# Kernel optimization log

Measured on AMD Instinct MI355X. Metric: run time of the kernel, lower is better.

Reference implementation:

```python
import jax, jax.numpy as jnp
import numpy as np

INV_SQRT2 = 0.7071067811865476  # 1/sqrt(2), orthonormal Haar
N_LEVELS = 3


def setup_inputs() -> dict:
    key = jax.random.key(0)
    ks = jax.random.split(key, 5)
    B, S, D = 16, 4096, 512
    x = jax.random.normal(ks[0], (B, S, D), dtype=jnp.float32)
    sizes = [256, 128, 64]  # detail-band sizes for 3-level DWT of 512
    Wd0 = jax.random.normal(ks[1], (sizes[0], sizes[0]), dtype=jnp.float32) * 0.02
    Wd1 = jax.random.normal(ks[2], (sizes[1], sizes[1]), dtype=jnp.float32) * 0.02
    Wd2 = jax.random.normal(ks[3], (sizes[2], sizes[2]), dtype=jnp.float32) * 0.02
    Wa = jax.random.normal(ks[4], (sizes[2], sizes[2]), dtype=jnp.float32) * 0.02
    return {
        'x': x,
        'Wd0': Wd0, 'bd0': jnp.zeros((sizes[0],), jnp.float32),
        'Wd1': Wd1, 'bd1': jnp.zeros((sizes[1],), jnp.float32),
        'Wd2': Wd2, 'bd2': jnp.zeros((sizes[2],), jnp.float32),
        'Wa': Wa, 'ba': jnp.zeros((sizes[2],), jnp.float32),
    }


def reference(x, Wd0, bd0, Wd1, bd1, Wd2, bd2, Wa, ba):
    # Multi-level Haar DWT along the feature axis.
    details = []
    a = x
    for _ in range(N_LEVELS):
        e = a[..., 0::2]
        o = a[..., 1::2]
        details.append((e - o) * INV_SQRT2)  # detail coefficients
        a = (e + o) * INV_SQRT2              # approximation coefficients

    # Per-level small linear transforms (torch Linear: y = x @ W.T + b).
    Wds, bds = [Wd0, Wd1, Wd2], [bd0, bd1, bd2]
    details = [details[i] @ Wds[i].T + bds[i] for i in range(N_LEVELS)]
    a = a @ Wa.T + ba

    # Inverse Haar DWT (orthonormal): even=(a+d)/sqrt2, odd=(a-d)/sqrt2, interleave.
    for i in reversed(range(N_LEVELS)):
        d = details[i]
        e = (a + d) * INV_SQRT2
        o = (a - d) * INV_SQRT2
        a = jnp.stack([e, o], axis=-1).reshape(a.shape[:-1] + (a.shape[-1] * 2,))
    return a
```

## Files before the change

### kernel.cpp

```cpp
#include <hip/hip_runtime.h>
#include <stdint.h>

typedef float  f32x4  __attribute__((ext_vector_type(4)));
typedef short  bf16x8 __attribute__((ext_vector_type(8)));
typedef int    i32x4  __attribute__((ext_vector_type(4)));
typedef unsigned int u32x2 __attribute__((ext_vector_type(2)));

#define C1f 0.70710678118654752f
#define C2f 0.5f
#define C3f 0.35355339059327373f

#define NT 1024
#define CH 32
#define RB 1040
#define RPB 256
#define NCHUNK (RPB/CH)

__device__ __forceinline__ unsigned int f2b(float f) {
    unsigned int u; __builtin_memcpy(&u, &f, 4);
    u += 0x7fffu + ((u >> 16) & 1u);
    return u >> 16;
}
__device__ __forceinline__ unsigned int pack2(float lo, float hi) {
    return f2b(lo) | (f2b(hi) << 16);
}
__device__ __forceinline__ bf16x8 cast8(i32x4 v) {
    bf16x8 r; __builtin_memcpy(&r, &v, 16); return r;
}

__device__ __forceinline__ void lds_barrier() {
    asm volatile("s_waitcnt lgkmcnt(0)" ::: "memory");
    __builtin_amdgcn_s_barrier();
    __builtin_amdgcn_sched_barrier(0);
}

__device__ __forceinline__ bf16x8 g_frag(int o, int i0,
        const float* __restrict__ W0, const float* __restrict__ W1,
        const float* __restrict__ W2, const float* __restrict__ Wa)
{
    const float s0o = (o & 1) ? -1.f : 1.f;
    const float s1o = ((o >> 1) & 1) ? -1.f : 1.f;
    const float s2o = ((o >> 2) & 1) ? -1.f : 1.f;
    const float4 w0 = *(const float4*)(W0 + (o >> 1) * 256 + (i0 >> 1));
    const float2 w1 = *(const float2*)(W1 + (o >> 2) * 128 + (i0 >> 2));
    const float  w2 = W2[(o >> 3) * 64 + (i0 >> 3)];
    const float  wa = Wa[(o >> 3) * 64 + (i0 >> 3)];
    const float base = 0.125f * wa;
    const float c2   = 0.125f * s2o * w2;
    const float c1   = 0.25f  * s1o;
    const float c0   = 0.5f   * s0o;
    const float w0a[4] = { w0.x, w0.y, w0.z, w0.w };
    const float w1a[2] = { w1.x, w1.y };
    float g[8];
    #pragma unroll
    for (int e = 0; e < 8; ++e) {
        const float t2 = ((e >> 2) & 1) ? -c2 : c2;
        const float t1 = (((e >> 1) & 1) ? -c1 : c1) * w1a[e >> 2];
        const float t0 = ((e & 1) ? -c0 : c0) * w0a[e >> 1];
        g[e] = base + t2 + t1 + t0;
    }
    i32x4 p = { (int)pack2(g[0],g[1]), (int)pack2(g[2],g[3]),
                (int)pack2(g[4],g[5]), (int)pack2(g[6],g[7]) };
    return cast8(p);
}

__global__ void prep(const float* __restrict__ W0, const float* __restrict__ b0,
                     const float* __restrict__ W1, const float* __restrict__ b1,
                     const float* __restrict__ W2, const float* __restrict__ b2,
                     const float* __restrict__ Wa, const float* __restrict__ ba,
                     unsigned short* __restrict__ ws)
{
    const int gid  = blockIdx.x * 256 + threadIdx.x;
    const int blob = gid >> 6, lane = gid & 63;
    const int otg  = blob >> 4, ks = blob & 15;
    const int o  = otg * 16 + (lane & 15);
    const int i0 = ks * 32 + ((lane >> 4) * 8);
    bf16x8 f = g_frag(o, i0, W0, W1, W2, Wa);
    i32x4 p; __builtin_memcpy(&p, &f, 16);
    *(i32x4*)(ws + blob * 512 + lane * 8) = p;
    if (gid < 512) {
        float* gv = (float*)(ws + 262144);
        const int oo = gid;
        const float s0 = (oo & 1) ? -C1f : C1f;
        const float s1 = ((oo >> 1) & 1) ? -C2f : C2f;
        const float s2 = ((oo >> 2) & 1) ? -C3f : C3f;
        gv[oo] = C3f * ba[oo >> 3] + s2 * b2[oo >> 3] + s1 * b1[oo >> 2] + s0 * b0[oo >> 1];
    }
}

template<int USE_WS>
__global__ __launch_bounds__(NT, 4)
void wavelet_gemm(const float* __restrict__ x,
                  const float* __restrict__ W0, const float* __restrict__ b0,
                  const float* __restrict__ W1, const float* __restrict__ b1,
                  const float* __restrict__ W2, const float* __restrict__ b2,
                  const float* __restrict__ Wa, const float* __restrict__ ba,
                  const unsigned short* __restrict__ wsb,
                  float* __restrict__ out)
{
    __shared__ char lds[2 * CH * RB];

    const int tid  = threadIdx.x;
    const int lane = tid & 63;
    const int wave = tid >> 6;
    const int bid  = blockIdx.x;
    const int chalf = bid & 1;
    const long rowblk = (long)(bid >> 1) * RPB;
    const int otg  = chalf * 16 + wave;
    const int col0 = otg * 16;
    const int bc0  = col0 + ((lane >> 4) << 2);

    bf16x8 B[16];
    if (USE_WS) {
        #pragma unroll
        for (int ks = 0; ks < 16; ++ks)
            B[ks] = cast8(*(const i32x4*)(wsb + ((size_t)(otg * 16 + ks) * 512) + lane * 8));
    } else {
        #pragma unroll
        for (int ks = 0; ks < 16; ++ks)
            B[ks] = g_frag(col0 + (lane & 15), ks * 32 + ((lane >> 4) * 8), W0, W1, W2, Wa);
    }
    #pragma unroll
    for (int ks = 0; ks < 16; ++ks) {
        i32x4 t; __builtin_memcpy(&t, &B[ks], 16);
        asm volatile("" : "+v"(t));
        __builtin_memcpy(&B[ks], &t, 16);
    }

    f32x4 gv4;
    if (USE_WS) {
        const float4 g4 = *(const float4*)((const float*)(wsb + 262144) + bc0);
        gv4 = f32x4{ g4.x, g4.y, g4.z, g4.w };
    } else {
        #pragma unroll
        for (int j = 0; j < 4; ++j) {
            const int col = bc0 + j;
            const float s0 = (col & 1) ? -C1f : C1f;
            const float s1 = ((col >> 1) & 1) ? -C2f : C2f;
            const float s2 = ((col >> 2) & 1) ? -C3f : C3f;
            gv4[j] = C3f * ba[col >> 3] + s2 * b2[col >> 3] + s1 * b1[col >> 2] + s0 * b0[col >> 1];
        }
    }

    auto ldx = [&](int c, f32x4* v) {
        const f32x4* xb = (const f32x4*)(x + (rowblk + (long)c * CH) * 512);
        #pragma unroll
        for (int i = 0; i < 4; ++i) v[i] = xb[i * NT + tid];
    };
    auto stx = [&](int b, const f32x4* v) {
        char* base = lds + b * (CH * RB);
        #pragma unroll
        for (int i = 0; i < 4; ++i) {
            const int f = i * NT + tid;
            const int row = f >> 7, c4 = f & 127;
            u32x2 p = { pack2(v[i][0], v[i][1]), pack2(v[i][2], v[i][3]) };
            *(u32x2*)(base + row * RB + c4 * 8) = p;
        }
    };
    auto compute = [&](int b, int c) {
        const char* base = lds + b * (CH * RB);
        const char* pa0 = base + (lane & 15) * RB + ((lane >> 4) * 16);
        const char* pa1 = pa0 + 16 * RB;
        f32x4 acc0 = {}, acc1 = {};
        #pragma unroll
        for (int ks = 0; ks < 16; ++ks) {
            bf16x8 a0 = cast8(*(const i32x4*)(pa0 + ks * 64));
            bf16x8 a1 = cast8(*(const i32x4*)(pa1 + ks * 64));
            acc0 = __builtin_amdgcn_mfma_f32_16x16x32_bf16(B[ks], a0, acc0, 0, 0, 0);
            acc1 = __builtin_amdgcn_mfma_f32_16x16x32_bf16(B[ks], a1, acc1, 0, 0, 0);
        }
        const long r0 = rowblk + (long)c * CH + (lane & 15);
        *(f32x4*)(out + r0 * 512 + bc0)        = acc0 + gv4;
        *(f32x4*)(out + (r0 + 16) * 512 + bc0) = acc1 + gv4;
    };

    {
        f32x4 v[4];
        ldx(0, v);
        stx(0, v);
    }
    lds_barrier();
    #pragma unroll 1
    for (int c = 0; c < NCHUNK; ++c) {
        f32x4 vn[4];
        if (c < NCHUNK - 1) ldx(c + 1, vn);
        compute(c & 1, c);
        if (c < NCHUNK - 1) stx((c + 1) & 1, vn);
        lds_barrier();
    }
}

extern "C" void kernel_launch(void* const* d_in, const int* in_sizes, int n_in,
                              void* d_out, int out_size, void* d_ws, size_t ws_size,
                              hipStream_t stream)
{
    const float* x  = (const float*)d_in[0];
    const float* W0 = (const float*)d_in[1];
    const float* b0 = (const float*)d_in[2];
    const float* W1 = (const float*)d_in[3];
    const float* b1 = (const float*)d_in[4];
    const float* W2 = (const float*)d_in[5];
    const float* b2 = (const float*)d_in[6];
    const float* Wa = (const float*)d_in[7];
    const float* ba = (const float*)d_in[8];
    float* out = (float*)d_out;

    const int nrows = in_sizes[0] / 512;
    const int nblk  = (nrows / RPB) * 2;

    if (ws_size >= (size_t)(524288 + 2048)) {
        unsigned short* ws = (unsigned short*)d_ws;
        prep<<<128, 256, 0, stream>>>(W0, b0, W1, b1, W2, b2, Wa, ba, ws);
        wavelet_gemm<1><<<nblk, NT, 0, stream>>>(x, W0, b0, W1, b1, W2, b2, Wa, ba, ws, out);
    } else {
        wavelet_gemm<0><<<nblk, NT, 0, stream>>>(x, W0, b0, W1, b1, W2, b2, Wa, ba, nullptr, out);
    }
}
```

Before: 77.90 us.

## Halve chunk size and prefetch two chunks ahead with vmcnt-controlled waits

Shrinks each LDS chunk from 32 to 16 rows and uses a four-slot LDS ring. Global loads are issued two chunks ahead, with explicit s_waitcnt vmcnt counts, so loads stay in flight across compute. The aim is deeper latency hiding of x loads behind MFMA work. The cost is a barrier per 16 rows, twice as many as before, and less MFMA work per barrier. The hand-counted vmcnt values also have to account for the output stores, which are vector memory operations too.

```diff
diff --git a/kernel.cpp b/kernel.cpp
--- a/kernel.cpp
+++ b/kernel.cpp
@@ -11,8 +11,9 @@
 #define C3f 0.35355339059327373f
 
 #define NT 1024
-#define CH 32
+#define CH 16
 #define RB 1040
+#define CHSZ (CH*RB)
 #define RPB 256
 #define NCHUNK (RPB/CH)
 
@@ -33,6 +34,9 @@
     __builtin_amdgcn_s_barrier();
     __builtin_amdgcn_sched_barrier(0);
 }
+__device__ __forceinline__ void vwait1() { asm volatile("s_waitcnt vmcnt(1)" ::: "memory"); __builtin_amdgcn_sched_barrier(0); }
+__device__ __forceinline__ void vwait2() { asm volatile("s_waitcnt vmcnt(2)" ::: "memory"); __builtin_amdgcn_sched_barrier(0); }
+__device__ __forceinline__ void vwait3() { asm volatile("s_waitcnt vmcnt(3)" ::: "memory"); __builtin_amdgcn_sched_barrier(0); }
 
 __device__ __forceinline__ bf16x8 g_frag(int o, int i0,
         const float* __restrict__ W0, const float* __restrict__ W1,
@@ -98,7 +102,7 @@
                   const unsigned short* __restrict__ wsb,
                   float* __restrict__ out)
 {
-    __shared__ char lds[2 * CH * RB];
+    __shared__ char lds[4 * CHSZ];
 
     const int tid  = threadIdx.x;
     const int lane = tid & 63;
@@ -144,48 +148,51 @@
 
     auto ldx = [&](int c, f32x4* v) {
         const f32x4* xb = (const f32x4*)(x + (rowblk + (long)c * CH) * 512);
-        #pragma unroll
-        for (int i = 0; i < 4; ++i) v[i] = xb[i * NT + tid];
+        v[0] = xb[tid];
+        v[1] = xb[NT + tid];
     };
-    auto stx = [&](int b, const f32x4* v) {
-        char* base = lds + b * (CH * RB);
-        #pragma unroll
-        for (int i = 0; i < 4; ++i) {
+    auto stx = [&](int c, const f32x4* v) {
+        char* base = lds + (c & 3) * CHSZ;
+        #pragma unroll
+        for (int i = 0; i < 2; ++i) {
             const int f = i * NT + tid;
             const int row = f >> 7, c4 = f & 127;
             u32x2 p = { pack2(v[i][0], v[i][1]), pack2(v[i][2], v[i][3]) };
             *(u32x2*)(base + row * RB + c4 * 8) = p;
         }
     };
-    auto compute = [&](int b, int c) {
-        const char* base = lds + b * (CH * RB);
-        const char* pa0 = base + (lane & 15) * RB + ((lane >> 4) * 16);
-        const char* pa1 = pa0 + 16 * RB;
-        f32x4 acc0 = {}, acc1 = {};
+    auto compute = [&](int c) {
+        const char* pa = lds + (c & 3) * CHSZ + (lane & 15) * RB + ((lane >> 4) * 16);
+        f32x4 acc = {};
         #pragma unroll
         for (int ks = 0; ks < 16; ++ks) {
-            bf16x8 a0 = cast8(*(const i32x4*)(pa0 + ks * 64));
-            bf16x8 a1 = cast8(*(const i32x4*)(pa1 + ks * 64));
-            acc0 = __builtin_amdgcn_mfma_f32_16x16x32_bf16(B[ks], a0, acc0, 0, 0, 0);
-            acc1 = __builtin_amdgcn_mfma_f32_16x16x32_bf16(B[ks], a1, acc1, 0, 0, 0);
+            bf16x8 a = cast8(*(const i32x4*)(pa + ks * 64));
+            acc = __builtin_amdgcn_mfma_f32_16x16x32_bf16(B[ks], a, acc, 0, 0, 0);
         }
         const long r0 = rowblk + (long)c * CH + (lane & 15);
-        *(f32x4*)(out + r0 * 512 + bc0)        = acc0 + gv4;
-        *(f32x4*)(out + (r0 + 16) * 512 + bc0) = acc1 + gv4;
+        *(f32x4*)(out + r0 * 512 + bc0) = acc + gv4;
     };
 
-    {
-        f32x4 v[4];
-        ldx(0, v);
-        stx(0, v);
-    }
+    f32x4 vA[2], vB2[2];
+    ldx(0, vA);
+    ldx(1, vB2);
+    vwait2();
+    stx(0, vA);
     lds_barrier();
+
     #pragma unroll 1
-    for (int c = 0; c < NCHUNK; ++c) {
-        f32x4 vn[4];
-        if (c < NCHUNK - 1) ldx(c + 1, vn);
-        compute(c & 1, c);
-        if (c < NCHUNK - 1) stx((c + 1) & 1, vn);
+    for (int cc = 0; cc < NCHUNK; cc += 2) {
+        compute(cc);
+        if (cc + 2 < NCHUNK) { ldx(cc + 2, vA); vwait3(); }
+        else                 { vwait1(); }
+        stx(cc + 1, vB2);
+        lds_barrier();
+        compute(cc + 1);
+        if (cc + 2 < NCHUNK) {
+            if (cc + 3 < NCHUNK) { ldx(cc + 3, vB2); vwait3(); }
+            else                 { vwait1(); }
+            stx(cc + 2, vA);
+        }
         lds_barrier();
     }
 }
```

New measurement: 81.85 us. 1.05x slower.
